# Kernel optimization log

Measured on AMD Instinct MI355X. Metric: run time of the kernel, lower is better.

Reference implementation:

```python
import jax, jax.numpy as jnp
import numpy as np

NUM_BINS = 31  # default num_bins in SummaryStats.from_array
N = 64 * 1024 * 1024  # 64M elements, 256 MB fp32 -> memory-bound reductions


def setup_inputs() -> dict:
    key = jax.random.key(0)
    x = jax.random.normal(key, (N,), dtype=jnp.float32)
    return {"x": x}


def reference(x):
    # SummaryStats.from_sharded_array on a single device (spec is fully replicated,
    # so _single_shard_histogram_array semantics apply: last bin is right-inclusive,
    # which matches jnp.histogram / searchsorted binning).
    x = x.ravel()
    mn = x.min()
    mx = x.max()
    nonzero_count = jnp.count_nonzero(x)
    num = jnp.asarray(x.size, dtype=nonzero_count.dtype)
    s = x.sum()
    ss = (x ** 2).sum()

    # histogram_bin_edges on stack([min, max]) with bins=NUM_BINS -> linspace(min, max, NUM_BINS+1)
    edges = jnp.linspace(mn, mx, NUM_BINS + 1)
    # bin index: values in [edges[i], edges[i+1]), last bin inclusive of edges[-1].
    idx = jnp.clip(jnp.searchsorted(edges, x, side="right") - 1, 0, NUM_BINS - 1)
    # exclude values strictly outside [min, max] (none here, but faithful to the compare logic)
    valid = (x >= edges[0]) & (x <= edges[-1])
    counts = jnp.zeros((NUM_BINS,), dtype=jnp.int32).at[idx].add(
        valid.astype(jnp.int32)
    )
    return mn, mx, num, nonzero_count, s, ss, counts, edges
```

## Files before the change

### kernel.cpp

```cpp
#include <hip/hip_runtime.h>

#define NBINS 31
#define NB1 2048
#define NB2 1024
#define PITCH 256

struct Partial {
    unsigned int mnk, mxk, nz, pad;
    double s, ss;
};
struct Finals {
    unsigned int minkey, maxkey;
    unsigned long long nz;
    double sum, ss;
};
#define OFF_F (NB1 * 32)
#define OFF_C (OFF_F + 64)

__device__ __forceinline__ unsigned int fkey(float f) {
    unsigned int u = __float_as_uint(f);
    return (u & 0x80000000u) ? ~u : (u | 0x80000000u);
}
__device__ __forceinline__ float funkey(unsigned int k) {
    return (k & 0x80000000u) ? __uint_as_float(k & 0x7FFFFFFFu)
                             : __uint_as_float(~k);
}
__device__ __forceinline__ float edge_at(float mn, float step, int i) {
    return __fadd_rn(mn, __fmul_rn((float)i, step));
}

__device__ __forceinline__ void acc4(float4 v, float& mn, float& mx, float& s, float& ss,
                                     unsigned int& nz) {
    mn = fminf(mn, fminf(fminf(v.x, v.y), fminf(v.z, v.w)));
    mx = fmaxf(mx, fmaxf(fmaxf(v.x, v.y), fmaxf(v.z, v.w)));
    s  += (v.x + v.y) + (v.z + v.w);
    ss += (v.x * v.x + v.y * v.y) + (v.z * v.z + v.w * v.w);
    nz += (v.x != 0.f) + (v.y != 0.f) + (v.z != 0.f) + (v.w != 0.f);
}

__global__ void __launch_bounds__(256) k_reduce(const float* __restrict__ x, long long n,
                                                Partial* __restrict__ part) {
    long long n4 = n >> 2;
    const float4* __restrict__ x4 = (const float4*)x;
    float mn = INFINITY, mx = -INFINITY, s = 0.f, ss = 0.f;
    unsigned int nz = 0u;

    long long stride = (long long)gridDim.x * blockDim.x;
    long long i = (long long)blockIdx.x * blockDim.x + threadIdx.x;
    for (; i + 3 * stride < n4; i += 4 * stride) {
        float4 a = x4[i], b = x4[i + stride], c = x4[i + 2 * stride], d = x4[i + 3 * stride];
        acc4(a, mn, mx, s, ss, nz);
        acc4(b, mn, mx, s, ss, nz);
        acc4(c, mn, mx, s, ss, nz);
        acc4(d, mn, mx, s, ss, nz);
    }
    for (; i < n4; i += stride) acc4(x4[i], mn, mx, s, ss, nz);
    if (blockIdx.x == 0 && threadIdx.x < (int)(n & 3)) {
        float v = x[(n4 << 2) + threadIdx.x];
        mn = fminf(mn, v); mx = fmaxf(mx, v);
        s += v; ss += v * v; nz += (v != 0.f);
    }

    double sd = (double)s, ssd = (double)ss;
    #pragma unroll
    for (int off = 32; off > 0; off >>= 1) {
        mn = fminf(mn, __shfl_down(mn, off));
        mx = fmaxf(mx, __shfl_down(mx, off));
        sd  += __shfl_down(sd, off);
        ssd += __shfl_down(ssd, off);
        nz  += __shfl_down(nz, off);
    }
    __shared__ float lmn[4], lmx[4];
    __shared__ double lsum[4], lss[4];
    __shared__ unsigned int lnz[4];
    int w = threadIdx.x >> 6;
    if ((threadIdx.x & 63) == 0) { lmn[w] = mn; lmx[w] = mx; lsum[w] = sd; lss[w] = ssd; lnz[w] = nz; }
    __syncthreads();
    if (threadIdx.x == 0) {
        Partial p;
        p.mnk = fkey(fminf(fminf(lmn[0], lmn[1]), fminf(lmn[2], lmn[3])));
        p.mxk = fkey(fmaxf(fmaxf(lmx[0], lmx[1]), fmaxf(lmx[2], lmx[3])));
        p.nz  = lnz[0] + lnz[1] + lnz[2] + lnz[3];
        p.pad = 0;
        p.s  = lsum[0] + lsum[1] + lsum[2] + lsum[3];
        p.ss = lss[0] + lss[1] + lss[2] + lss[3];
        part[blockIdx.x] = p;
    }
}

__global__ void __launch_bounds__(256) k_mid(const Partial* __restrict__ part,
                                             Finals* __restrict__ fin) {
    unsigned int mnk = 0xFFFFFFFFu, mxk = 0u;
    unsigned long long nz = 0ull;
    double s = 0.0, ss = 0.0;
    for (int i = threadIdx.x; i < NB1; i += 256) {
        Partial p = part[i];
        mnk = min(mnk, p.mnk); mxk = max(mxk, p.mxk);
        nz += p.nz; s += p.s; ss += p.ss;
    }
    #pragma unroll
    for (int off = 32; off > 0; off >>= 1) {
        mnk = min(mnk, __shfl_down(mnk, off));
        mxk = max(mxk, __shfl_down(mxk, off));
        nz += __shfl_down(nz, off);
        s  += __shfl_down(s, off);
        ss += __shfl_down(ss, off);
    }
    __shared__ unsigned int la[4], lb[4];
    __shared__ unsigned long long lnz[4];
    __shared__ double ls[4], lss[4];
    int w = threadIdx.x >> 6;
    if ((threadIdx.x & 63) == 0) { la[w] = mnk; lb[w] = mxk; lnz[w] = nz; ls[w] = s; lss[w] = ss; }
    __syncthreads();
    if (threadIdx.x == 0) {
        fin->minkey = min(min(la[0], la[1]), min(la[2], la[3]));
        fin->maxkey = max(max(lb[0], lb[1]), max(lb[2], lb[3]));
        fin->nz  = lnz[0] + lnz[1] + lnz[2] + lnz[3];
        fin->sum = ls[0] + ls[1] + ls[2] + ls[3];
        fin->ss  = lss[0] + lss[1] + lss[2] + lss[3];
    }
}

__device__ __forceinline__ void bump(float v, float mn, float inv,
                                     const float* __restrict__ E,
                                     unsigned int* __restrict__ hist, int tid) {
    int b = (int)((v - mn) * inv);
    b = b > 30 ? 30 : b;
    float lo = E[b];
    float hi = E[b + 1];
    b += (v >= hi);
    b -= (v < lo);
    b = b > 30 ? 30 : b;
    atomicAdd(&hist[(b << 8) + tid], 1u);
}

__global__ void __launch_bounds__(256) k_hist(const float* __restrict__ x, long long n,
                                              const Finals* __restrict__ fin,
                                              unsigned int* __restrict__ cpart) {
    __shared__ unsigned int hist[NBINS * PITCH];
    __shared__ float E[NBINS + 1];
    int tid = threadIdx.x;
    for (int j = tid; j < NBINS * PITCH; j += 256) hist[j] = 0u;

    float mn = funkey(fin->minkey);
    float mx = funkey(fin->maxkey);
    float step = (mx - mn) / 31.0f;
    float inv  = 31.0f / (mx - mn);
    if (tid < NBINS + 1) E[tid] = (tid == NBINS) ? mx : edge_at(mn, step, tid);
    __syncthreads();

    long long n4 = n >> 2;
    const float4* __restrict__ x4 = (const float4*)x;
    long long stride = (long long)gridDim.x * blockDim.x;
    long long i = (long long)blockIdx.x * blockDim.x + tid;
    for (; i + stride < n4; i += 2 * stride) {
        float4 a = x4[i], b = x4[i + stride];
        bump(a.x, mn, inv, E, hist, tid); bump(a.y, mn, inv, E, hist, tid);
        bump(a.z, mn, inv, E, hist, tid); bump(a.w, mn, inv, E, hist, tid);
        bump(b.x, mn, inv, E, hist, tid); bump(b.y, mn, inv, E, hist, tid);
        bump(b.z, mn, inv, E, hist, tid); bump(b.w, mn, inv, E, hist, tid);
    }
    for (; i < n4; i += stride) {
        float4 a = x4[i];
        bump(a.x, mn, inv, E, hist, tid); bump(a.y, mn, inv, E, hist, tid);
        bump(a.z, mn, inv, E, hist, tid); bump(a.w, mn, inv, E, hist, tid);
    }
    if (blockIdx.x == 0 && tid < (int)(n & 3))
        bump(x[(n4 << 2) + tid], mn, inv, E, hist, tid);
    __syncthreads();

    int w = tid >> 6, lane = tid & 63;
    for (int b = w; b < NBINS; b += 4) {
        const unsigned int* row = &hist[b * PITCH];
        uint4 q = *(const uint4*)(row + (lane << 2));
        unsigned int sv = q.x + q.y + q.z + q.w;
        #pragma unroll
        for (int off = 32; off > 0; off >>= 1) sv += __shfl_down(sv, off);
        if (lane == 0) cpart[b * NB2 + blockIdx.x] = sv;
    }
}

__global__ void __launch_bounds__(256) k_final(const Finals* __restrict__ fin,
                                               const unsigned int* __restrict__ cpart,
                                               float* __restrict__ out, long long n) {
    float mn = funkey(fin->minkey);
    float mx = funkey(fin->maxkey);
    float step = (mx - mn) / 31.0f;
    int w = threadIdx.x >> 6, lane = threadIdx.x & 63;
    for (int b = w; b < NBINS; b += 4) {
        const uint4* row = (const uint4*)(cpart + b * NB2);
        unsigned int sv = 0;
        for (int k = lane; k < NB2 / 4; k += 64) {
            uint4 q = row[k];
            sv += q.x + q.y + q.z + q.w;
        }
        #pragma unroll
        for (int off = 32; off > 0; off >>= 1) sv += __shfl_down(sv, off);
        if (lane == 0) out[6 + b] = (float)sv;
    }
    int t = threadIdx.x;
    if (t == 0) {
        out[0] = mn;
        out[1] = mx;
        out[2] = (float)n;
        out[3] = (float)fin->nz;
        out[4] = (float)fin->sum;
        out[5] = (float)fin->ss;
    }
    if (t < NBINS + 1) out[6 + NBINS + t] = (t == NBINS) ? mx : edge_at(mn, step, t);
}

extern "C" void kernel_launch(void* const* d_in, const int* in_sizes, int n_in,
                              void* d_out, int out_size, void* d_ws, size_t ws_size,
                              hipStream_t stream) {
    const float* x = (const float*)d_in[0];
    long long n = (long long)in_sizes[0];
    char* ws = (char*)d_ws;
    Partial* part = (Partial*)ws;
    Finals* fin = (Finals*)(ws + OFF_F);
    unsigned int* cpart = (unsigned int*)(ws + OFF_C);
    float* out = (float*)d_out;

    k_reduce<<<dim3(NB1), dim3(256), 0, stream>>>(x, n, part);
    k_mid<<<dim3(1), dim3(256), 0, stream>>>(part, fin);
    k_hist<<<dim3(NB2), dim3(256), 0, stream>>>(x, n, fin, cpart);
    k_final<<<dim3(1), dim3(256), 0, stream>>>(fin, cpart, out, n);
}
```

Before: 421.5 us.

## Fuse four kernels into one cooperative kernel with grid syncs and reversed histogram pass

Replaces the reduce, mid, histogram and final kernels with a single cooperative kernel of 512 blocks that uses grid.sync between phases. Every block redundantly reduces the per-block partials to get min/max instead of running a separate single-block kernel. The histogram pass walks each thread's range in reverse so the data read last by the reduction pass is reused from cache (MI355X has a large Infinity Cache). This removes launch gaps and may reduce HBM traffic for the second read, at the cost of grid-sync overhead and a fixed grid size that must fit as co-resident blocks.

```diff
diff --git a/kernel.cpp b/kernel.cpp
--- a/kernel.cpp
+++ b/kernel.cpp
@@ -1,21 +1,17 @@
 #include <hip/hip_runtime.h>
+#include <hip/hip_cooperative_groups.h>
+namespace cg = cooperative_groups;
 
 #define NBINS 31
-#define NB1 2048
-#define NB2 1024
+#define NB 512
+#define NT 256
 #define PITCH 256
 
 struct Partial {
     unsigned int mnk, mxk, nz, pad;
     double s, ss;
 };
-struct Finals {
-    unsigned int minkey, maxkey;
-    unsigned long long nz;
-    double sum, ss;
-};
-#define OFF_F (NB1 * 32)
-#define OFF_C (OFF_F + 64)
+#define OFF_C (NB * 32)
 
 __device__ __forceinline__ unsigned int fkey(float f) {
     unsigned int u = __float_as_uint(f);
@@ -36,89 +32,6 @@
     s  += (v.x + v.y) + (v.z + v.w);
     ss += (v.x * v.x + v.y * v.y) + (v.z * v.z + v.w * v.w);
     nz += (v.x != 0.f) + (v.y != 0.f) + (v.z != 0.f) + (v.w != 0.f);
-}
-
-__global__ void __launch_bounds__(256) k_reduce(const float* __restrict__ x, long long n,
-                                                Partial* __restrict__ part) {
-    long long n4 = n >> 2;
-    const float4* __restrict__ x4 = (const float4*)x;
-    float mn = INFINITY, mx = -INFINITY, s = 0.f, ss = 0.f;
-    unsigned int nz = 0u;
-
-    long long stride = (long long)gridDim.x * blockDim.x;
-    long long i = (long long)blockIdx.x * blockDim.x + threadIdx.x;
-    for (; i + 3 * stride < n4; i += 4 * stride) {
-        float4 a = x4[i], b = x4[i + stride], c = x4[i + 2 * stride], d = x4[i + 3 * stride];
-        acc4(a, mn, mx, s, ss, nz);
-        acc4(b, mn, mx, s, ss, nz);
-        acc4(c, mn, mx, s, ss, nz);
-        acc4(d, mn, mx, s, ss, nz);
-    }
-    for (; i < n4; i += stride) acc4(x4[i], mn, mx, s, ss, nz);
-    if (blockIdx.x == 0 && threadIdx.x < (int)(n & 3)) {
-        float v = x[(n4 << 2) + threadIdx.x];
-        mn = fminf(mn, v); mx = fmaxf(mx, v);
-        s += v; ss += v * v; nz += (v != 0.f);
-    }
-
-    double sd = (double)s, ssd = (double)ss;
-    #pragma unroll
-    for (int off = 32; off > 0; off >>= 1) {
-        mn = fminf(mn, __shfl_down(mn, off));
-        mx = fmaxf(mx, __shfl_down(mx, off));
-        sd  += __shfl_down(sd, off);
-        ssd += __shfl_down(ssd, off);
-        nz  += __shfl_down(nz, off);
-    }
-    __shared__ float lmn[4], lmx[4];
-    __shared__ double lsum[4], lss[4];
-    __shared__ unsigned int lnz[4];
-    int w = threadIdx.x >> 6;
-    if ((threadIdx.x & 63) == 0) { lmn[w] = mn; lmx[w] = mx; lsum[w] = sd; lss[w] = ssd; lnz[w] = nz; }
-    __syncthreads();
-    if (threadIdx.x == 0) {
-        Partial p;
-        p.mnk = fkey(fminf(fminf(lmn[0], lmn[1]), fminf(lmn[2], lmn[3])));
-        p.mxk = fkey(fmaxf(fmaxf(lmx[0], lmx[1]), fmaxf(lmx[2], lmx[3])));
-        p.nz  = lnz[0] + lnz[1] + lnz[2] + lnz[3];
-        p.pad = 0;
-        p.s  = lsum[0] + lsum[1] + lsum[2] + lsum[3];
-        p.ss = lss[0] + lss[1] + lss[2] + lss[3];
-        part[blockIdx.x] = p;
-    }
-}
-
-__global__ void __launch_bounds__(256) k_mid(const Partial* __restrict__ part,
-                                             Finals* __restrict__ fin) {
-    unsigned int mnk = 0xFFFFFFFFu, mxk = 0u;
-    unsigned long long nz = 0ull;
-    double s = 0.0, ss = 0.0;
-    for (int i = threadIdx.x; i < NB1; i += 256) {
-        Partial p = part[i];
-        mnk = min(mnk, p.mnk); mxk = max(mxk, p.mxk);
-        nz += p.nz; s += p.s; ss += p.ss;
-    }
-    #pragma unroll
-    for (int off = 32; off > 0; off >>= 1) {
-        mnk = min(mnk, __shfl_down(mnk, off));
-        mxk = max(mxk, __shfl_down(mxk, off));
-        nz += __shfl_down(nz, off);
-        s  += __shfl_down(s, off);
-        ss += __shfl_down(ss, off);
-    }
-    __shared__ unsigned int la[4], lb[4];
-    __shared__ unsigned long long lnz[4];
-    __shared__ double ls[4], lss[4];
-    int w = threadIdx.x >> 6;
-    if ((threadIdx.x & 63) == 0) { la[w] = mnk; lb[w] = mxk; lnz[w] = nz; ls[w] = s; lss[w] = ss; }
-    __syncthreads();
-    if (threadIdx.x == 0) {
-        fin->minkey = min(min(la[0], la[1]), min(la[2], la[3]));
-        fin->maxkey = max(max(lb[0], lb[1]), max(lb[2], lb[3]));
-        fin->nz  = lnz[0] + lnz[1] + lnz[2] + lnz[3];
-        fin->sum = ls[0] + ls[1] + ls[2] + ls[3];
-        fin->ss  = lss[0] + lss[1] + lss[2] + lss[3];
-    }
 }
 
 __device__ __forceinline__ void bump(float v, float mn, float inv,
@@ -134,80 +47,165 @@
     atomicAdd(&hist[(b << 8) + tid], 1u);
 }
 
-__global__ void __launch_bounds__(256) k_hist(const float* __restrict__ x, long long n,
-                                              const Finals* __restrict__ fin,
-                                              unsigned int* __restrict__ cpart) {
+__global__ void __launch_bounds__(NT) k_all(const float* __restrict__ x, long long n,
+                                            Partial* __restrict__ part,
+                                            unsigned int* __restrict__ cpart,
+                                            float* __restrict__ out) {
+    cg::grid_group grid = cg::this_grid();
     __shared__ unsigned int hist[NBINS * PITCH];
     __shared__ float E[NBINS + 1];
+    __shared__ float lmn[4], lmx[4];
+    __shared__ double lsum[4], lss2[4];
+    __shared__ unsigned long long lnz[4];
+    __shared__ float bmn, bmx;
+    __shared__ double bs, bss;
+    __shared__ unsigned long long bnz;
+
     int tid = threadIdx.x;
-    for (int j = tid; j < NBINS * PITCH; j += 256) hist[j] = 0u;
-
-    float mn = funkey(fin->minkey);
-    float mx = funkey(fin->maxkey);
+    int w = tid >> 6, lane = tid & 63;
+    long long n4 = n >> 2;
+    const float4* __restrict__ x4 = (const float4*)x;
+    long long stride = (long long)NB * NT;
+    long long base = (long long)blockIdx.x * NT + tid;
+
+    {
+        float mn = INFINITY, mx = -INFINITY, s = 0.f, ss = 0.f;
+        unsigned int nz = 0u;
+        long long i = base;
+        for (; i + 3 * stride < n4; i += 4 * stride) {
+            float4 a = x4[i], b = x4[i + stride], c = x4[i + 2 * stride], d = x4[i + 3 * stride];
+            acc4(a, mn, mx, s, ss, nz);
+            acc4(b, mn, mx, s, ss, nz);
+            acc4(c, mn, mx, s, ss, nz);
+            acc4(d, mn, mx, s, ss, nz);
+        }
+        for (; i < n4; i += stride) acc4(x4[i], mn, mx, s, ss, nz);
+        if (blockIdx.x == 0 && tid < (int)(n & 3)) {
+            float v = x[(n4 << 2) + tid];
+            mn = fminf(mn, v); mx = fmaxf(mx, v);
+            s += v; ss += v * v; nz += (v != 0.f);
+        }
+        double sd = (double)s, ssd = (double)ss;
+        #pragma unroll
+        for (int off = 32; off > 0; off >>= 1) {
+            mn = fminf(mn, __shfl_down(mn, off));
+            mx = fmaxf(mx, __shfl_down(mx, off));
+            sd  += __shfl_down(sd, off);
+            ssd += __shfl_down(ssd, off);
+            nz  += __shfl_down(nz, off);
+        }
+        if (lane == 0) { lmn[w] = mn; lmx[w] = mx; lsum[w] = sd; lss2[w] = ssd; lnz[w] = nz; }
+        __syncthreads();
+        if (tid == 0) {
+            Partial p;
+            p.mnk = fkey(fminf(fminf(lmn[0], lmn[1]), fminf(lmn[2], lmn[3])));
+            p.mxk = fkey(fmaxf(fmaxf(lmx[0], lmx[1]), fmaxf(lmx[2], lmx[3])));
+            p.nz  = (unsigned int)(lnz[0] + lnz[1] + lnz[2] + lnz[3]);
+            p.pad = 0;
+            p.s  = lsum[0] + lsum[1] + lsum[2] + lsum[3];
+            p.ss = lss2[0] + lss2[1] + lss2[2] + lss2[3];
+            part[blockIdx.x] = p;
+        }
+    }
+    for (int j = tid; j < NBINS * PITCH; j += NT) hist[j] = 0u;
+    __threadfence();
+    grid.sync();
+
+    {
+        unsigned int mnk = 0xFFFFFFFFu, mxk = 0u;
+        unsigned long long nz = 0ull;
+        double s = 0.0, ss = 0.0;
+        for (int i = tid; i < NB; i += NT) {
+            Partial p = part[i];
+            mnk = min(mnk, p.mnk); mxk = max(mxk, p.mxk);
+            nz += p.nz; s += p.s; ss += p.ss;
+        }
+        #pragma unroll
+        for (int off = 32; off > 0; off >>= 1) {
+            mnk = min(mnk, __shfl_down(mnk, off));
+            mxk = max(mxk, __shfl_down(mxk, off));
+            nz += __shfl_down(nz, off);
+            s  += __shfl_down(s, off);
+            ss += __shfl_down(ss, off);
+        }
+        __syncthreads();
+        if (lane == 0) {
+            lmn[w] = __uint_as_float(mnk); lmx[w] = __uint_as_float(mxk);
+            lsum[w] = s; lss2[w] = ss; lnz[w] = nz;
+        }
+        __syncthreads();
+        if (tid == 0) {
+            unsigned int a0 = min(min(__float_as_uint(lmn[0]), __float_as_uint(lmn[1])),
+                                  min(__float_as_uint(lmn[2]), __float_as_uint(lmn[3])));
+            unsigned int b0 = max(max(__float_as_uint(lmx[0]), __float_as_uint(lmx[1])),
+                                  max(__float_as_uint(lmx[2]), __float_as_uint(lmx[3])));
+            bmn = funkey(a0);
+            bmx = funkey(b0);
+            bs  = lsum[0] + lsum[1] + lsum[2] + lsum[3];
+            bss = lss2[0] + lss2[1] + lss2[2] + lss2[3];
+            bnz = lnz[0] + lnz[1] + lnz[2] + lnz[3];
+        }
+        __syncthreads();
+    }
+    float mn = bmn, mx = bmx;
     float step = (mx - mn) / 31.0f;
     float inv  = 31.0f / (mx - mn);
     if (tid < NBINS + 1) E[tid] = (tid == NBINS) ? mx : edge_at(mn, step, tid);
     __syncthreads();
 
-    long long n4 = n >> 2;
-    const float4* __restrict__ x4 = (const float4*)x;
-    long long stride = (long long)gridDim.x * blockDim.x;
-    long long i = (long long)blockIdx.x * blockDim.x + tid;
-    for (; i + stride < n4; i += 2 * stride) {
-        float4 a = x4[i], b = x4[i + stride];
-        bump(a.x, mn, inv, E, hist, tid); bump(a.y, mn, inv, E, hist, tid);
-        bump(a.z, mn, inv, E, hist, tid); bump(a.w, mn, inv, E, hist, tid);
-        bump(b.x, mn, inv, E, hist, tid); bump(b.y, mn, inv, E, hist, tid);
-        bump(b.z, mn, inv, E, hist, tid); bump(b.w, mn, inv, E, hist, tid);
-    }
-    for (; i < n4; i += stride) {
-        float4 a = x4[i];
-        bump(a.x, mn, inv, E, hist, tid); bump(a.y, mn, inv, E, hist, tid);
-        bump(a.z, mn, inv, E, hist, tid); bump(a.w, mn, inv, E, hist, tid);
+    if (base < n4) {
+        long long K = (n4 - 1 - base) / stride;
+        long long i = base + K * stride;
+        for (; i >= base + stride; i -= 2 * stride) {
+            float4 a = x4[i], b = x4[i - stride];
+            bump(a.x, mn, inv, E, hist, tid); bump(a.y, mn, inv, E, hist, tid);
+            bump(a.z, mn, inv, E, hist, tid); bump(a.w, mn, inv, E, hist, tid);
+            bump(b.x, mn, inv, E, hist, tid); bump(b.y, mn, inv, E, hist, tid);
+            bump(b.z, mn, inv, E, hist, tid); bump(b.w, mn, inv, E, hist, tid);
+        }
+        if (i >= base) {
+            float4 a = x4[i];
+            bump(a.x, mn, inv, E, hist, tid); bump(a.y, mn, inv, E, hist, tid);
+            bump(a.z, mn, inv, E, hist, tid); bump(a.w, mn, inv, E, hist, tid);
+        }
     }
     if (blockIdx.x == 0 && tid < (int)(n & 3))
         bump(x[(n4 << 2) + tid], mn, inv, E, hist, tid);
     __syncthreads();
 
-    int w = tid >> 6, lane = tid & 63;
     for (int b = w; b < NBINS; b += 4) {
         const unsigned int* row = &hist[b * PITCH];
         uint4 q = *(const uint4*)(row + (lane << 2));
         unsigned int sv = q.x + q.y + q.z + q.w;
         #pragma unroll
         for (int off = 32; off > 0; off >>= 1) sv += __shfl_down(sv, off);
-        if (lane == 0) cpart[b * NB2 + blockIdx.x] = sv;
-    }
-}
-
-__global__ void __launch_bounds__(256) k_final(const Finals* __restrict__ fin,
-                                               const unsigned int* __restrict__ cpart,
-                                               float* __restrict__ out, long long n) {
-    float mn = funkey(fin->minkey);
-    float mx = funkey(fin->maxkey);
-    float step = (mx - mn) / 31.0f;
-    int w = threadIdx.x >> 6, lane = threadIdx.x & 63;
-    for (int b = w; b < NBINS; b += 4) {
-        const uint4* row = (const uint4*)(cpart + b * NB2);
-        unsigned int sv = 0;
-        for (int k = lane; k < NB2 / 4; k += 64) {
-            uint4 q = row[k];
-            sv += q.x + q.y + q.z + q.w;
-        }
-        #pragma unroll
-        for (int off = 32; off > 0; off >>= 1) sv += __shfl_down(sv, off);
-        if (lane == 0) out[6 + b] = (float)sv;
-    }
-    int t = threadIdx.x;
-    if (t == 0) {
-        out[0] = mn;
-        out[1] = mx;
-        out[2] = (float)n;
-        out[3] = (float)fin->nz;
-        out[4] = (float)fin->sum;
-        out[5] = (float)fin->ss;
-    }
-    if (t < NBINS + 1) out[6 + NBINS + t] = (t == NBINS) ? mx : edge_at(mn, step, t);
+        if (lane == 0) cpart[b * NB + blockIdx.x] = sv;
+    }
+    __threadfence();
+    grid.sync();
+
+    if (blockIdx.x == 0) {
+        for (int b = w; b < NBINS; b += 4) {
+            const uint4* row = (const uint4*)(cpart + b * NB);
+            unsigned int sv = 0;
+            for (int k = lane; k < NB / 4; k += 64) {
+                uint4 q = row[k];
+                sv += q.x + q.y + q.z + q.w;
+            }
+            #pragma unroll
+            for (int off = 32; off > 0; off >>= 1) sv += __shfl_down(sv, off);
+            if (lane == 0) out[6 + b] = (float)sv;
+        }
+        if (tid == 0) {
+            out[0] = mn;
+            out[1] = mx;
+            out[2] = (float)n;
+            out[3] = (float)bnz;
+            out[4] = (float)bs;
+            out[5] = (float)bss;
+        }
+        if (tid < NBINS + 1) out[6 + NBINS + tid] = (tid == NBINS) ? mx : edge_at(mn, step, tid);
+    }
 }
 
 extern "C" void kernel_launch(void* const* d_in, const int* in_sizes, int n_in,
@@ -217,12 +215,9 @@
     long long n = (long long)in_sizes[0];
     char* ws = (char*)d_ws;
     Partial* part = (Partial*)ws;
-    Finals* fin = (Finals*)(ws + OFF_F);
     unsigned int* cpart = (unsigned int*)(ws + OFF_C);
     float* out = (float*)d_out;
 
-    k_reduce<<<dim3(NB1), dim3(256), 0, stream>>>(x, n, part);
-    k_mid<<<dim3(1), dim3(256), 0, stream>>>(part, fin);
-    k_hist<<<dim3(NB2), dim3(256), 0, stream>>>(x, n, fin, cpart);
-    k_final<<<dim3(1), dim3(256), 0, stream>>>(fin, cpart, out, n);
-}
+    void* args[] = {(void*)&x, (void*)&n, (void*)&part, (void*)&cpart, (void*)&out};
+    hipLaunchCooperativeKernel((const void*)k_all, dim3(NB), dim3(NT), args, 0, stream);
+}
```

Result: slower. 637.1 us (+51.2%).

## Traverse histogram pass in reverse to reuse cache-resident tail of reduce pass

Applied to the files above, without the earlier changes.

The histogram kernel now walks its grid-stride loop from the end of the array backward, so data most recently read by the reduction kernel is consumed first while it may still be in the last-level cache. The reduction loop is unrolled to eight float4 loads per iteration with compile-time grid stride, and the histogram grid grows from 1024 to 1280 blocks. This trades more per-block partial histograms and higher register use for less DRAM traffic on the second pass.

```diff
diff --git a/kernel.cpp b/kernel.cpp
--- a/kernel.cpp
+++ b/kernel.cpp
@@ -2,7 +2,7 @@
 
 #define NBINS 31
 #define NB1 2048
-#define NB2 1024
+#define NB2 1280
 #define PITCH 256
 
 struct Partial {
@@ -45,14 +45,17 @@
     float mn = INFINITY, mx = -INFINITY, s = 0.f, ss = 0.f;
     unsigned int nz = 0u;
 
-    long long stride = (long long)gridDim.x * blockDim.x;
-    long long i = (long long)blockIdx.x * blockDim.x + threadIdx.x;
-    for (; i + 3 * stride < n4; i += 4 * stride) {
-        float4 a = x4[i], b = x4[i + stride], c = x4[i + 2 * stride], d = x4[i + 3 * stride];
-        acc4(a, mn, mx, s, ss, nz);
-        acc4(b, mn, mx, s, ss, nz);
-        acc4(c, mn, mx, s, ss, nz);
-        acc4(d, mn, mx, s, ss, nz);
+    long long stride = (long long)NB1 * 256;
+    long long i = (long long)blockIdx.x * 256 + threadIdx.x;
+    for (; i + 7 * stride < n4; i += 8 * stride) {
+        float4 v0 = x4[i],              v1 = x4[i + stride];
+        float4 v2 = x4[i + 2 * stride], v3 = x4[i + 3 * stride];
+        float4 v4 = x4[i + 4 * stride], v5 = x4[i + 5 * stride];
+        float4 v6 = x4[i + 6 * stride], v7 = x4[i + 7 * stride];
+        acc4(v0, mn, mx, s, ss, nz); acc4(v1, mn, mx, s, ss, nz);
+        acc4(v2, mn, mx, s, ss, nz); acc4(v3, mn, mx, s, ss, nz);
+        acc4(v4, mn, mx, s, ss, nz); acc4(v5, mn, mx, s, ss, nz);
+        acc4(v6, mn, mx, s, ss, nz); acc4(v7, mn, mx, s, ss, nz);
     }
     for (; i < n4; i += stride) acc4(x4[i], mn, mx, s, ss, nz);
     if (blockIdx.x == 0 && threadIdx.x < (int)(n & 3)) {
@@ -151,19 +154,24 @@
 
     long long n4 = n >> 2;
     const float4* __restrict__ x4 = (const float4*)x;
-    long long stride = (long long)gridDim.x * blockDim.x;
-    long long i = (long long)blockIdx.x * blockDim.x + tid;
-    for (; i + stride < n4; i += 2 * stride) {
-        float4 a = x4[i], b = x4[i + stride];
-        bump(a.x, mn, inv, E, hist, tid); bump(a.y, mn, inv, E, hist, tid);
-        bump(a.z, mn, inv, E, hist, tid); bump(a.w, mn, inv, E, hist, tid);
-        bump(b.x, mn, inv, E, hist, tid); bump(b.y, mn, inv, E, hist, tid);
-        bump(b.z, mn, inv, E, hist, tid); bump(b.w, mn, inv, E, hist, tid);
-    }
-    for (; i < n4; i += stride) {
-        float4 a = x4[i];
-        bump(a.x, mn, inv, E, hist, tid); bump(a.y, mn, inv, E, hist, tid);
-        bump(a.z, mn, inv, E, hist, tid); bump(a.w, mn, inv, E, hist, tid);
+    long long stride = (long long)NB2 * 256;
+    long long base = (long long)blockIdx.x * 256 + tid;
+
+    if (base < n4) {
+        long long K = (n4 - 1 - base) / stride;
+        long long i = base + K * stride;
+        for (; i >= base + stride; i -= 2 * stride) {
+            float4 a = x4[i], b = x4[i - stride];
+            bump(a.x, mn, inv, E, hist, tid); bump(a.y, mn, inv, E, hist, tid);
+            bump(a.z, mn, inv, E, hist, tid); bump(a.w, mn, inv, E, hist, tid);
+            bump(b.x, mn, inv, E, hist, tid); bump(b.y, mn, inv, E, hist, tid);
+            bump(b.z, mn, inv, E, hist, tid); bump(b.w, mn, inv, E, hist, tid);
+        }
+        if (i >= base) {
+            float4 a = x4[i];
+            bump(a.x, mn, inv, E, hist, tid); bump(a.y, mn, inv, E, hist, tid);
+            bump(a.z, mn, inv, E, hist, tid); bump(a.w, mn, inv, E, hist, tid);
+        }
     }
     if (blockIdx.x == 0 && tid < (int)(n & 3))
         bump(x[(n4 << 2) + tid], mn, inv, E, hist, tid);
```

New measurement: 425.1 us. Within noise of the previous version (+0.9%).
